# Performance work log

Measured on AMD Instinct MI355X. Metric: run time of the kernel, lower is better.

Reference implementation:

```python
import jax, jax.numpy as jnp
import numpy as np

EMBED_DIM = 1024
HEAD_DIM = 64
B, T = 4, 4096


def setup_inputs() -> dict:
    key = jax.random.key(0)
    kx, kq, kk, kv = jax.random.split(key, 4)
    x = jax.random.normal(kx, (B, T, EMBED_DIM), dtype=jnp.float32)
    # nn.Linear weights, stored transposed as (in, out) for x @ W
    s = 1.0 / np.sqrt(EMBED_DIM)
    Wq = jax.random.normal(kq, (EMBED_DIM, HEAD_DIM), dtype=jnp.float32) * s
    Wk = jax.random.normal(kk, (EMBED_DIM, HEAD_DIM), dtype=jnp.float32) * s
    Wv = jax.random.normal(kv, (EMBED_DIM, HEAD_DIM), dtype=jnp.float32) * s
    return {"x": x, "Wq": Wq, "Wk": Wk, "Wv": Wv}


def reference(x, Wq, Wk, Wv):
    Bc, Tc, C = x.shape
    Q = x @ Wq  # [B, T, H]
    K = x @ Wk
    V = x @ Wv
    # NOTE: original scales by embedding_dim C, not head_dim
    scores = jnp.einsum('bqh,bkh->bqk', Q, K) / jnp.sqrt(jnp.float32(C))
    causal = jnp.tril(jnp.ones((Tc, Tc), dtype=bool))
    scores = jnp.where(causal, scores, -jnp.inf)
    attn = jax.nn.softmax(scores, axis=-1)
    return jnp.einsum('bqk,bkh->bqh', attn, V)
```

## Files before the change

kernel.cpp:

```cpp
#include <hip/hip_runtime.h>
#include <hip/hip_bf16.h>
#include <math.h>

typedef __attribute__((ext_vector_type(8))) short bf16x8;
typedef __attribute__((ext_vector_type(4))) float f32x4;

#define MFMA16 __builtin_amdgcn_mfma_f32_16x16x32_bf16

static constexpr int TSEQ = 4096;
static constexpr int EMB = 1024;
static constexpr int HD = 64;

__device__ __forceinline__ unsigned short f2bf(float f) {
    unsigned u = __builtin_bit_cast(unsigned, f);
    u += 0x7fffu + ((u >> 16) & 1u);
    return (unsigned short)(u >> 16);
}

__device__ __forceinline__ void gll16(const void* g, void* l) {
    __builtin_amdgcn_global_load_lds(
        (const __attribute__((address_space(1))) void*)g,
        (__attribute__((address_space(3))) void*)l, 16, 0, 0);
}

#define WAITV6 asm volatile("s_waitcnt vmcnt(6)" ::: "memory")
#define WAITV0 asm volatile("s_waitcnt vmcnt(0)" ::: "memory")
#define WAITLG asm volatile("s_waitcnt lgkmcnt(0)" ::: "memory")
__device__ __forceinline__ void barrier_sync() {
    asm volatile("" ::: "memory");
    __builtin_amdgcn_s_barrier();
    asm volatile("" ::: "memory");
}

__global__ void prep_w(const float* __restrict__ Wq, const float* __restrict__ Wk,
                       const float* __restrict__ Wv, unsigned short* __restrict__ Wp) {
    int id = blockIdx.x * 256 + threadIdx.x;
    int wsel = id >> 16;
    int t = id & 65535;
    int k = t >> 6, n0 = t & 63;
    const float* W = (wsel == 0) ? Wq : (wsel == 1) ? Wk : Wv;
    float v = W[t];
    if (wsel == 0) v *= 0.03125f;
    int n = wsel * 64 + n0;
    Wp[(k >> 5) * 6144 + (n >> 4) * 512 + ((k >> 3) & 3) * 128 + (n & 15) * 8 + (k & 7)] = f2bf(v);
}

__global__ __launch_bounds__(1024, 4) void proj_kernel(const float* __restrict__ X,
        const unsigned short* __restrict__ Wp, unsigned short* __restrict__ Qp,
        unsigned short* __restrict__ Kp, unsigned short* __restrict__ Vp) {
    __shared__ unsigned short wlds[3][12288];
    __shared__ unsigned short xlds[3][4096];

    const int tid = threadIdx.x;
    const int lane = tid & 63, wave = tid >> 6;
    const int col = lane & 15, quad = lane >> 4;
    const int mq = wave >> 2, nw = wave & 3;
    const int row0 = blockIdx.x * 64;

    f32x4 acc[3];
#pragma unroll
    for (int j = 0; j < 3; j++) acc[j] = (f32x4)(0.0f);

    const char* wsrc = (const char*)Wp + lane * 16;
    auto stageW = [&](int p, int b) {
        char* d = (char*)wlds + b * 24576;
#pragma unroll
        for (int u = 0; u < 2; u++) {
            const char* s = wsrc + (size_t)(2 * p + u) * 12288;
            char* du = d + u * 12288;
            gll16(s + wave * 1024,       du + wave * 1024);
            gll16(s + (4 + wave) * 1024, du + (4 + wave) * 1024);
            gll16(s + (8 + wave) * 1024, du + (8 + wave) * 1024);
        }
    };
    const int u2 = tid - 256;
    const int xrow = u2 >> 3, q8 = u2 & 7;
    const bool xstager = (wave >= 4) && (wave < 12);
    const float* xsrc = xstager ? (X + (size_t)(row0 + xrow) * EMB + q8 * 8) : X;
    const int xo = (q8 >> 2) * 4096 + (xrow >> 4) * 1024 + (q8 & 3) * 256 + (xrow & 15) * 16;

    auto wr8 = [&](int b, float4 f0, float4 f1) {
        union { unsigned short s[8]; bf16x8 v; } r;
        r.s[0] = f2bf(f0.x); r.s[1] = f2bf(f0.y); r.s[2] = f2bf(f0.z); r.s[3] = f2bf(f0.w);
        r.s[4] = f2bf(f1.x); r.s[5] = f2bf(f1.y); r.s[6] = f2bf(f1.z); r.s[7] = f2bf(f1.w);
        *(bf16x8*)((char*)xlds + b * 8192 + xo) = r.v;
    };
    auto compute = [&](int b) {
        bf16x8 A[2], Wf[2][3];
        const char* xb = (const char*)xlds + b * 8192;
        const char* wb = (const char*)wlds + b * 24576;
#pragma unroll
        for (int u = 0; u < 2; u++) {
            A[u] = *(const bf16x8*)(xb + u * 4096 + mq * 1024 + lane * 16);
#pragma unroll
            for (int j = 0; j < 3; j++)
                Wf[u][j] = *(const bf16x8*)(wb + u * 12288 + (j * 4 + nw) * 1024 + lane * 16);
        }
#pragma unroll
        for (int u = 0; u < 2; u++)
#pragma unroll
            for (int j = 0; j < 3; j++)
                acc[j] = MFMA16(A[u], Wf[u][j], acc[j], 0, 0, 0);
    };

    int bc = 0, bx = 1, bw = 2;
    float4 pa0, pa1, qa0, qa1;

    if (wave < 4) {
        stageW(0, 0);
        stageW(1, 1);
        WAITV6;
    } else if (xstager) {
        float4 t0 = *(const float4*)(xsrc);
        float4 t1 = *(const float4*)(xsrc + 4);
        wr8(0, t0, t1);
        pa0 = *(const float4*)(xsrc + 64);
        pa1 = *(const float4*)(xsrc + 68);
        WAITLG;
    }
    barrier_sync();

    auto step = [&](int s, float4& w0, float4& w1, float4& l0, float4& l1) {
        if (wave < 4) {
            if (s + 2 < 16) stageW(s + 2, bw);
        } else if (xstager) {
            if (s + 2 < 16) {
                l0 = *(const float4*)(xsrc + (s + 2) * 64);
                l1 = *(const float4*)(xsrc + (s + 2) * 64 + 4);
            }
            if (s + 1 < 16) wr8(bx, w0, w1);
        }
        compute(bc);
        if (wave < 4) {
            if (s + 2 < 16) { WAITV6; } else { WAITV0; }
        } else if (xstager) {
            WAITLG;
        }
        barrier_sync();
        int t = bc; bc = bx; bx = bw; bw = t;
    };

    for (int si = 0; si < 8; si++) {
        step(2 * si,     pa0, pa1, qa0, qa1);
        step(2 * si + 1, qa0, qa1, pa0, pa1);
    }

    const int t = blockIdx.x * 4 + mq;
#pragma unroll
    for (int r = 0; r < 4; r++)
        Qp[t * 1024 + (nw >> 1) * 512 + (quad * 4 + r) * 32 +
           ((nw & 1) * 2 + (col >> 3)) * 8 + (col & 7)] = f2bf(acc[0][r]);
#pragma unroll
    for (int r = 0; r < 4; r++)
        Kp[(t * 2 + (nw >> 1)) * 512 + (quad * 4 + r) * 32 +
           ((nw & 1) * 2 + (col >> 3)) * 8 + (col & 7)] = f2bf(acc[1][r]);
    {
        ushort4 pk;
        pk.x = f2bf(acc[2][0]); pk.y = f2bf(acc[2][1]);
        pk.z = f2bf(acc[2][2]); pk.w = f2bf(acc[2][3]);
        *(ushort4*)&Vp[(t >> 1) * 2048 + nw * 512 + col * 32 + (t & 1) * 16 + quad * 4] = pk;
    }
}

__global__ __launch_bounds__(512, 4) void attn_kernel(const unsigned short* __restrict__ Qp,
        const unsigned short* __restrict__ Kp, const unsigned short* __restrict__ Vp,
        float* __restrict__ Out) {
    __shared__ float cmb[4][2][64][20];
    __shared__ unsigned short plds[8][2][640];
    const int lane = threadIdx.x & 63, wave = threadIdx.x >> 6;
    const int col = lane & 15, quad = lane >> 4;
    const int batch = blockIdx.x & 3;
    const int ti = 127 - (blockIdx.x >> 2);
    const int q0 = ti * 32;
    const size_t bT = (size_t)batch * TSEQ;
    const int fragoff = col * 64 + quad * 16;

    const char* QpB = (const char*)Qp;
    const char* KpB = (const char*)Kp;
    const char* VpB = (const char*)Vp;
    const int gt = (int)((bT + q0) >> 4);
    const int c0 = (int)(bT >> 5);

    bf16x8 aq[2][2];
#pragma unroll
    for (int m = 0; m < 2; m++)
#pragma unroll
        for (int h = 0; h < 2; h++)
            aq[m][h] = *(const bf16x8*)(QpB + (size_t)((gt + m) * 2 + h) * 1024 + fragoff);

    f32x4 o[2][4];
    f32x4 lsum[2];
#pragma unroll
    for (int m = 0; m < 2; m++) {
        lsum[m] = (f32x4)(0.0f);
#pragma unroll
        for (int t = 0; t < 4; t++) o[m][t] = (f32x4)(0.0f);
    }

    for (int c = wave; c <= ti; c += 8) {
        const char* kb = KpB + (size_t)(c0 + c) * 4096;
        const char* vb = VpB + (size_t)(c0 + c) * 4096;
        bf16x8 bk[2][2], bv[4];
#pragma unroll
        for (int j = 0; j < 2; j++)
#pragma unroll
            for (int h = 0; h < 2; h++)
                bk[j][h] = *(const bf16x8*)(kb + j * 2048 + h * 1024 + fragoff);
#pragma unroll
        for (int t = 0; t < 4; t++)
            bv[t] = *(const bf16x8*)(vb + t * 1024 + fragoff);

        f32x4 s[2][2];
#pragma unroll
        for (int m = 0; m < 2; m++)
#pragma unroll
            for (int j = 0; j < 2; j++) {
                f32x4 a = MFMA16(aq[m][0], bk[j][0], (f32x4)(0.0f), 0, 0, 0);
                s[m][j] = MFMA16(aq[m][1], bk[j][1], a, 0, 0, 0);
            }
        const bool diag = (c == ti);
#pragma unroll
        for (int m = 0; m < 2; m++)
#pragma unroll
            for (int j = 0; j < 2; j++)
#pragma unroll
                for (int r = 0; r < 4; r++) {
                    float v = s[m][j][r];
                    if (diag && (j * 16 + col > m * 16 + quad * 4 + r)) v = -INFINITY;
                    const float p = __expf(v);
                    lsum[m][r] += p;
                    plds[wave][m][(quad * 4 + r) * 40 + j * 16 + col] =
                        (unsigned short)(__builtin_bit_cast(unsigned, p) >> 16);
                }
        bf16x8 pa[2];
#pragma unroll
        for (int m = 0; m < 2; m++)
            pa[m] = *(const bf16x8*)(&plds[wave][m][col * 40 + quad * 8]);
#pragma unroll
        for (int m = 0; m < 2; m++)
#pragma unroll
            for (int t = 0; t < 4; t++)
                o[m][t] = MFMA16(pa[m], bv[t], o[m][t], 0, 0, 0);
    }

    auto wr = [&](int s) {
#pragma unroll
        for (int m = 0; m < 2; m++) {
#pragma unroll
            for (int t = 0; t < 4; t++)
                *(f32x4*)&cmb[s][m][lane][t * 4] = o[m][t];
            *(f32x4*)&cmb[s][m][lane][16] = lsum[m];
        }
    };
    auto rd = [&](int s) {
#pragma unroll
        for (int m = 0; m < 2; m++) {
#pragma unroll
            for (int t = 0; t < 4; t++)
                o[m][t] += *(const f32x4*)&cmb[s][m][lane][t * 4];
            lsum[m] += *(const f32x4*)&cmb[s][m][lane][16];
        }
    };
    if (wave >= 4) wr(wave - 4);
    __syncthreads();
    if (wave < 4) rd(wave);
    __syncthreads();
    if (wave == 2 || wave == 3) wr(wave);
    __syncthreads();
    if (wave < 2) rd(wave + 2);
    __syncthreads();
    if (wave == 1) wr(1);
    __syncthreads();
    if (wave == 0) {
        rd(1);
#pragma unroll
        for (int off = 1; off < 16; off <<= 1)
#pragma unroll
            for (int m = 0; m < 2; m++)
#pragma unroll
                for (int r = 0; r < 4; r++)
                    lsum[m][r] += __shfl_xor(lsum[m][r], off, 64);
#pragma unroll
        for (int m = 0; m < 2; m++)
#pragma unroll
            for (int r = 0; r < 4; r++) {
                const float inv = 1.0f / lsum[m][r];
                const size_t orow = (bT + q0 + m * 16 + quad * 4 + r) * HD;
#pragma unroll
                for (int t = 0; t < 4; t++)
                    Out[orow + t * 16 + col] = o[m][t][r] * inv;
            }
    }
}

extern "C" void kernel_launch(void* const* d_in, const int* in_sizes, int n_in,
                              void* d_out, int out_size, void* d_ws, size_t ws_size,
                              hipStream_t stream) {
    const float* x  = (const float*)d_in[0];
    const float* Wq = (const float*)d_in[1];
    const float* Wk = (const float*)d_in[2];
    const float* Wv = (const float*)d_in[3];
    float* out = (float*)d_out;

    char* w = (char*)d_ws;
    unsigned short* Wp = (unsigned short*)(w);
    unsigned short* Qp = (unsigned short*)(w + (512 << 10));
    unsigned short* Kp = (unsigned short*)(w + (512 << 10) + (2 << 20));
    unsigned short* Vp = (unsigned short*)(w + (512 << 10) + (4 << 20));

    hipLaunchKernelGGL(prep_w, dim3(768), dim3(256), 0, stream, Wq, Wk, Wv, Wp);
    hipLaunchKernelGGL(proj_kernel, dim3(256), dim3(1024), 0, stream, x, Wp, Qp, Kp, Vp);
    hipLaunchKernelGGL(attn_kernel, dim3(512), dim3(512), 0, stream, Qp, Kp, Vp, out);
}
```

Before: 137.8 us.

## Process 64 query rows per attention block to halve K/V reloads

Each attention block now covers 64 query rows (four 16-row tiles) instead of 32, so every K/V chunk loaded from memory feeds twice as many score MFMAs. The diagonal chunk is handled with a relative causal mask, and the top two query tiles are skipped for the last chunk. Shared memory is pooled and reused between the P staging buffer and the cross-wave reduction, and two waves now finalize outputs in parallel. The grid is halved and launch bounds lowered to 2 blocks per SM, which trades occupancy and more registers for better data reuse. Blocks no longer run in reverse order, so the largest causal blocks are not scheduled first.

```diff
diff --git a/kernel.cpp b/kernel.cpp
--- a/kernel.cpp
+++ b/kernel.cpp
@@ -162,16 +162,20 @@
     }
 }
 
-__global__ __launch_bounds__(512, 4) void attn_kernel(const unsigned short* __restrict__ Qp,
+__global__ __launch_bounds__(512, 2) void attn_kernel(const unsigned short* __restrict__ Qp,
         const unsigned short* __restrict__ Kp, const unsigned short* __restrict__ Vp,
         float* __restrict__ Out) {
-    __shared__ float cmb[4][2][64][20];
-    __shared__ unsigned short plds[8][2][640];
+    __shared__ __align__(16) char pool[81920];
+    auto cmb  = (float (*)[4][64][20])pool;
+    auto plds = (unsigned short (*)[4][640])pool;
+
     const int lane = threadIdx.x & 63, wave = threadIdx.x >> 6;
     const int col = lane & 15, quad = lane >> 4;
     const int batch = blockIdx.x & 3;
-    const int ti = 127 - (blockIdx.x >> 2);
-    const int q0 = ti * 32;
+    const int tb = blockIdx.x >> 2;
+    const int q0 = tb * 64;
+    const int tb2 = tb * 2;
+    const int cmax = tb2 + 1;
     const size_t bT = (size_t)batch * TSEQ;
     const int fragoff = col * 64 + quad * 16;
 
@@ -181,23 +185,23 @@
     const int gt = (int)((bT + q0) >> 4);
     const int c0 = (int)(bT >> 5);
 
-    bf16x8 aq[2][2];
-#pragma unroll
-    for (int m = 0; m < 2; m++)
+    bf16x8 aq[4][2];
+#pragma unroll
+    for (int m = 0; m < 4; m++)
 #pragma unroll
         for (int h = 0; h < 2; h++)
             aq[m][h] = *(const bf16x8*)(QpB + (size_t)((gt + m) * 2 + h) * 1024 + fragoff);
 
-    f32x4 o[2][4];
-    f32x4 lsum[2];
-#pragma unroll
-    for (int m = 0; m < 2; m++) {
+    f32x4 o[4][4];
+    f32x4 lsum[4];
+#pragma unroll
+    for (int m = 0; m < 4; m++) {
         lsum[m] = (f32x4)(0.0f);
 #pragma unroll
         for (int t = 0; t < 4; t++) o[m][t] = (f32x4)(0.0f);
     }
 
-    for (int c = wave; c <= ti; c += 8) {
+    for (int c = wave; c <= cmax; c += 8) {
         const char* kb = KpB + (size_t)(c0 + c) * 4096;
         const char* vb = VpB + (size_t)(c0 + c) * 4096;
         bf16x8 bk[2][2], bv[4];
@@ -210,57 +214,83 @@
         for (int t = 0; t < 4; t++)
             bv[t] = *(const bf16x8*)(vb + t * 1024 + fragoff);
 
-        f32x4 s[2][2];
-#pragma unroll
-        for (int m = 0; m < 2; m++)
+        const int crel = c - tb2;
+        const bool skipm01 = (crel >= 1);
+        const bool haveMask = (crel >= 0);
+
+        f32x4 s[4][2];
+#pragma unroll
+        for (int m = 0; m < 4; m++) {
+            if (skipm01 && m < 2) continue;
 #pragma unroll
             for (int j = 0; j < 2; j++) {
                 f32x4 a = MFMA16(aq[m][0], bk[j][0], (f32x4)(0.0f), 0, 0, 0);
                 s[m][j] = MFMA16(aq[m][1], bk[j][1], a, 0, 0, 0);
             }
-        const bool diag = (c == ti);
-#pragma unroll
-        for (int m = 0; m < 2; m++)
+        }
+#pragma unroll
+        for (int m = 0; m < 4; m++) {
+            if (skipm01 && m < 2) continue;
 #pragma unroll
             for (int j = 0; j < 2; j++)
 #pragma unroll
                 for (int r = 0; r < 4; r++) {
                     float v = s[m][j][r];
-                    if (diag && (j * 16 + col > m * 16 + quad * 4 + r)) v = -INFINITY;
+                    if (haveMask && (crel * 32 + j * 16 + col > m * 16 + quad * 4 + r))
+                        v = -INFINITY;
                     const float p = __expf(v);
                     lsum[m][r] += p;
                     plds[wave][m][(quad * 4 + r) * 40 + j * 16 + col] =
                         (unsigned short)(__builtin_bit_cast(unsigned, p) >> 16);
                 }
-        bf16x8 pa[2];
-#pragma unroll
-        for (int m = 0; m < 2; m++)
-            pa[m] = *(const bf16x8*)(&plds[wave][m][col * 40 + quad * 8]);
-#pragma unroll
-        for (int m = 0; m < 2; m++)
+        }
+#pragma unroll
+        for (int m = 0; m < 4; m++) {
+            if (skipm01 && m < 2) continue;
+            bf16x8 pa = *(const bf16x8*)(&plds[wave][m][col * 40 + quad * 8]);
 #pragma unroll
             for (int t = 0; t < 4; t++)
-                o[m][t] = MFMA16(pa[m], bv[t], o[m][t], 0, 0, 0);
-    }
-
+                o[m][t] = MFMA16(pa, bv[t], o[m][t], 0, 0, 0);
+        }
+    }
+
+    auto wr1 = [&](int s, int m) {
+#pragma unroll
+        for (int t = 0; t < 4; t++)
+            *(f32x4*)&cmb[s][m][lane][t * 4] = o[m][t];
+        *(f32x4*)&cmb[s][m][lane][16] = lsum[m];
+    };
+    auto rd1 = [&](int s, int m) {
+#pragma unroll
+        for (int t = 0; t < 4; t++)
+            o[m][t] += *(const f32x4*)&cmb[s][m][lane][t * 4];
+        lsum[m] += *(const f32x4*)&cmb[s][m][lane][16];
+    };
     auto wr = [&](int s) {
 #pragma unroll
-        for (int m = 0; m < 2; m++) {
+        for (int m = 0; m < 4; m++) wr1(s, m);
+    };
+    auto rd = [&](int s) {
+#pragma unroll
+        for (int m = 0; m < 4; m++) rd1(s, m);
+    };
+    auto finalize = [&](int m) {
+#pragma unroll
+        for (int off = 1; off < 16; off <<= 1)
+#pragma unroll
+            for (int r = 0; r < 4; r++)
+                lsum[m][r] += __shfl_xor(lsum[m][r], off, 64);
+#pragma unroll
+        for (int r = 0; r < 4; r++) {
+            const float inv = 1.0f / lsum[m][r];
+            const size_t orow = (bT + q0 + m * 16 + quad * 4 + r) * HD;
 #pragma unroll
             for (int t = 0; t < 4; t++)
-                *(f32x4*)&cmb[s][m][lane][t * 4] = o[m][t];
-            *(f32x4*)&cmb[s][m][lane][16] = lsum[m];
-        }
-    };
-    auto rd = [&](int s) {
-#pragma unroll
-        for (int m = 0; m < 2; m++) {
-#pragma unroll
-            for (int t = 0; t < 4; t++)
-                o[m][t] += *(const f32x4*)&cmb[s][m][lane][t * 4];
-            lsum[m] += *(const f32x4*)&cmb[s][m][lane][16];
-        }
-    };
+                Out[orow + t * 16 + col] = o[m][t][r] * inv;
+        }
+    };
+
+    __syncthreads();
     if (wave >= 4) wr(wave - 4);
     __syncthreads();
     if (wave < 4) rd(wave);
@@ -269,27 +299,15 @@
     __syncthreads();
     if (wave < 2) rd(wave + 2);
     __syncthreads();
-    if (wave == 1) wr(1);
+    if (wave == 1) { wr1(0, 0); wr1(0, 1); }
+    if (wave == 0) { wr1(1, 2); wr1(1, 3); }
     __syncthreads();
     if (wave == 0) {
-        rd(1);
-#pragma unroll
-        for (int off = 1; off < 16; off <<= 1)
-#pragma unroll
-            for (int m = 0; m < 2; m++)
-#pragma unroll
-                for (int r = 0; r < 4; r++)
-                    lsum[m][r] += __shfl_xor(lsum[m][r], off, 64);
-#pragma unroll
-        for (int m = 0; m < 2; m++)
-#pragma unroll
-            for (int r = 0; r < 4; r++) {
-                const float inv = 1.0f / lsum[m][r];
-                const size_t orow = (bT + q0 + m * 16 + quad * 4 + r) * HD;
-#pragma unroll
-                for (int t = 0; t < 4; t++)
-                    Out[orow + t * 16 + col] = o[m][t][r] * inv;
-            }
+        rd1(0, 0); rd1(0, 1);
+        finalize(0); finalize(1);
+    } else if (wave == 1) {
+        rd1(1, 2); rd1(1, 3);
+        finalize(2); finalize(3);
     }
 }
 
@@ -310,5 +328,5 @@
 
     hipLaunchKernelGGL(prep_w, dim3(768), dim3(256), 0, stream, Wq, Wk, Wv, Wp);
     hipLaunchKernelGGL(proj_kernel, dim3(256), dim3(1024), 0, stream, x, Wp, Qp, Kp, Vp);
-    hipLaunchKernelGGL(attn_kernel, dim3(512), dim3(512), 0, stream, Qp, Kp, Vp, out);
-}
+    hipLaunchKernelGGL(attn_kernel, dim3(256), dim3(512), 0, stream, Qp, Kp, Vp, out);
+}
```

Measured after the change: 144.3 us. 4.7% more time.
